# Kernel optimization log

Measured on AMD Instinct MI355X. Metric: run time of the kernel, lower is better.

Reference implementation:

```python
import jax, jax.numpy as jnp
import numpy as np

N_NODES = 50000
N_EDGES = 1600000
N_FEAT = 128
EMB = 128
N_CLASSES = 10
N_GRAPHS = 512


def setup_inputs() -> dict:
    key = jax.random.key(0)
    ks = jax.random.split(key, 12)
    x = jax.random.normal(ks[0], (N_NODES, N_FEAT), dtype=jnp.float32)
    edge_index = jax.random.randint(ks[1], (2, N_EDGES), 0, N_NODES, dtype=jnp.int64)
    batch = jnp.sort(jax.random.randint(ks[2], (N_NODES,), 0, N_GRAPHS, dtype=jnp.int64))
    def glorot(k, fan_in, fan_out):
        lim = jnp.sqrt(6.0 / (fan_in + fan_out)).astype(jnp.float32)
        return jax.random.uniform(k, (fan_in, fan_out), jnp.float32, -lim, lim)
    W0 = glorot(ks[3], N_FEAT, EMB); b0 = jnp.zeros((EMB,), jnp.float32)
    W1 = glorot(ks[4], EMB, EMB);    b1 = jnp.zeros((EMB,), jnp.float32)
    W2 = glorot(ks[5], EMB, EMB);    b2 = jnp.zeros((EMB,), jnp.float32)
    Wout = glorot(ks[6], EMB, N_CLASSES)
    bout = jnp.zeros((N_CLASSES,), jnp.float32)
    return {"x": x, "edge_index": edge_index, "batch": batch,
            "W0": W0, "b0": b0, "W1": W1, "b1": b1, "W2": W2, "b2": b2,
            "Wout": Wout, "bout": bout}


def _gcn_conv(x, W, b, src, dst, norm, n_nodes):
    # PyG GCNConv: h = x @ W; aggregate norm * h[src] into dst; add bias.
    h = x @ W                                  # [N, out]
    msg = h[src] * norm[:, None]               # [E+N, out] gather (incl. self-loops)
    out = jax.ops.segment_sum(msg, dst, num_segments=n_nodes)
    return out + b


def reference(x, edge_index, batch, W0, b0, W1, b1, W2, b2, Wout, bout):
    n_nodes = x.shape[0]
    # add self-loops (GCNConv default add_self_loops=True)
    loops = jnp.arange(n_nodes, dtype=edge_index.dtype)
    src = jnp.concatenate([edge_index[0], loops])
    dst = jnp.concatenate([edge_index[1], loops])
    # symmetric normalization D^{-1/2} (A+I) D^{-1/2}
    deg = jax.ops.segment_sum(jnp.ones_like(dst, dtype=x.dtype), dst,
                              num_segments=n_nodes)
    deg_inv_sqrt = jnp.where(deg > 0, jax.lax.rsqrt(jnp.maximum(deg, 1.0)), 0.0)
    norm = deg_inv_sqrt[src] * deg_inv_sqrt[dst]   # [E+N]
    out = jnp.tanh(_gcn_conv(x, W0, b0, src, dst, norm, n_nodes))
    out = jnp.tanh(_gcn_conv(out, W1, b1, src, dst, norm, n_nodes))
    out = _gcn_conv(out, W2, b2, src, dst, norm, n_nodes)
    # global mean pool over per-node graph ids
    sums = jax.ops.segment_sum(out, batch, num_segments=N_GRAPHS)
    counts = jax.ops.segment_sum(jnp.ones((n_nodes,), out.dtype), batch,
                                 num_segments=N_GRAPHS)
    pooled = sums / jnp.maximum(counts, 1.0)[:, None]   # [G, EMB]
    logits = pooled @ Wout + bout                        # [G, C]
    return jax.nn.log_softmax(logits, axis=1)
```

## Files before the change

### kernel.cpp

```cpp
#include <hip/hip_runtime.h>
#include <math.h>


#define BLK_EDGES 4096
#define MAXB 128
#define ECAP 2048
#define NPB 8
#define WS_STRIDE 136

typedef __attribute__((ext_vector_type(8))) short bf16x8;
typedef __attribute__((ext_vector_type(4))) float f32x4;
typedef __attribute__((ext_vector_type(2))) float f32x2;

static __device__ inline unsigned short f2bf(float f) {
    unsigned u = __float_as_uint(f);
    unsigned r = (u + 0x7FFFu + ((u >> 16) & 1u)) >> 16;
    return (unsigned short)r;
}
static __device__ inline float bf_lo(unsigned u) { return __uint_as_float(u << 16); }
static __device__ inline float bf_hi(unsigned u) { return __uint_as_float(u & 0xFFFF0000u); }
static __device__ inline unsigned char f2fp8(float v) {
    v = fminf(fmaxf(v, -240.f), 240.f);
    int u = __builtin_amdgcn_cvt_pk_fp8_f32(v, v, 0, false);
    return (unsigned char)(u & 0xFF);
}

__global__ __launch_bounds__(256) void blk_hist_prep(const int* __restrict__ dst,
        int* __restrict__ histT, int E, int NBLK, int NB,
        const float* __restrict__ W0, const float* __restrict__ W1,
        const float* __restrict__ W2, unsigned short* __restrict__ wt0,
        unsigned short* __restrict__ wt1, unsigned short* __restrict__ wt2) {
    __shared__ int h[MAXB];
    int blk = blockIdx.x, t = threadIdx.x;
    if (blk >= NBLK) {
        int i = (blk - NBLK) * 256 + t;
        int w = i >> 14, j = i & 16383;
        int k = j >> 7, n2 = j & 127;
        const float* Wp = (w == 0) ? W0 : (w == 1) ? W1 : W2;
        unsigned short* Wt = (w == 0) ? wt0 : (w == 1) ? wt1 : wt2;
        Wt[n2 * 128 + k] = f2bf(Wp[k * 128 + n2]);
        return;
    }
    for (int i = t; i < NB; i += 256) h[i] = 0;
    __syncthreads();
    int lo = blk * BLK_EDGES;
    int hi = min(E, lo + BLK_EDGES);
    for (int i = lo + t; i < hi; i += 256)
        atomicAdd(&h[dst[i] >> 9], 1);
    __syncthreads();
    for (int i = t; i < NB; i += 256) histT[i * NBLK + blk] = h[i];
}

__global__ void scan_block(const int* __restrict__ cnt, int* __restrict__ off,
                           int* __restrict__ bsum, int n) {
    __shared__ int lds[256];
    int t = threadIdx.x;
    int i = blockIdx.x * 256 + t;
    int v = (i < n) ? cnt[i] : 0;
    lds[t] = v;
    __syncthreads();
    for (int d = 1; d < 256; d <<= 1) {
        int add = (t >= d) ? lds[t - d] : 0;
        __syncthreads();
        lds[t] += add;
        __syncthreads();
    }
    if (i < n) off[i] = lds[t] - v;
    if (t == 255) bsum[blockIdx.x] = lds[255];
}

__global__ void scan_top(const int* __restrict__ bsum, int* __restrict__ boff,
                         int nblocks) {
    __shared__ int lds[256];
    int t = threadIdx.x;
    int v = (t < nblocks) ? bsum[t] : 0;
    lds[t] = v;
    __syncthreads();
    for (int d = 1; d < 256; d <<= 1) {
        int add = (t >= d) ? lds[t - d] : 0;
        __syncthreads();
        lds[t] += add;
        __syncthreads();
    }
    if (t < nblocks) boff[t] = lds[t] - v;
}

__global__ __launch_bounds__(256) void scatter_packed(const int* __restrict__ src,
        const int* __restrict__ dst, const int* __restrict__ P,
        const int* __restrict__ boff, unsigned* __restrict__ packed,
        int E, int NBLK, int NB) {
    __shared__ int cur[MAXB];
    int blk = blockIdx.x, t = threadIdx.x;
    for (int i = t; i < NB; i += 256) {
        int idx = i * NBLK + blk;
        cur[i] = P[idx] + boff[idx >> 8];
    }
    __syncthreads();
    int lo = blk * BLK_EDGES;
    int hi = min(E, lo + BLK_EDGES);
    for (int i = lo + t; i < hi; i += 256) {
        int d = dst[i];
        int pos = atomicAdd(&cur[d >> 9], 1);
        packed[pos] = ((unsigned)d << 16) | (unsigned)src[i];
    }
}

__global__ __launch_bounds__(256) void bucket_build(const unsigned* __restrict__ packed,
        const int* __restrict__ P, const int* __restrict__ boff, int* __restrict__ off,
        float* __restrict__ dis, unsigned short* __restrict__ csr16,
        int E, int NBLK, int N, int NB) {
    __shared__ int cnt[512];
    __shared__ int loc[512];
    __shared__ int ps[256];
    int b = blockIdx.x, t = threadIdx.x;
    int i0 = b * NBLK, i1 = (b + 1) * NBLK;
    int start = P[i0] + boff[i0 >> 8];
    int end   = (b == NB - 1) ? E : (P[i1] + boff[i1 >> 8]);
    cnt[t] = 0; cnt[t + 256] = 0;
    __syncthreads();
    for (int i = start + t; i < end; i += 256)
        atomicAdd(&cnt[(packed[i] >> 16) & 511], 1);
    __syncthreads();
    int c0 = cnt[2 * t], c1 = cnt[2 * t + 1];
    ps[t] = c0 + c1;
    __syncthreads();
    for (int d = 1; d < 256; d <<= 1) {
        int add = (t >= d) ? ps[t - d] : 0;
        __syncthreads();
        ps[t] += add;
        __syncthreads();
    }
    int pexcl = ps[t] - (c0 + c1);
    loc[2 * t]     = start + pexcl;
    loc[2 * t + 1] = start + pexcl + c0;
    __syncthreads();
    int node0 = b * 512;
    for (int l = t; l < 512; l += 256) {
        int node = node0 + l;
        if (node < N) {
            off[node] = loc[l];
            dis[node] = rsqrtf((float)cnt[l] + 1.0f);
        }
    }
    if (b == NB - 1 && t == 0) off[N] = E;
    __syncthreads();
    for (int i = start + t; i < end; i += 256) {
        unsigned p = packed[i];
        int l = (p >> 16) & 511;
        int pos = atomicAdd(&loc[l], 1);
        csr16[pos] = (unsigned short)(p & 0xFFFFu);
    }
}

template<int IN_F32>
__global__ __launch_bounds__(128) void gemm_mfma(const void* __restrict__ Av,
        const unsigned short* __restrict__ Wt, const float* __restrict__ dis,
        unsigned char* __restrict__ Hs8, int n) {
    __shared__ unsigned short Ws[128 * WS_STRIDE];
    int t = threadIdx.x;
    for (int i = t; i < 128 * 16; i += 128) {
        int r = i >> 4, j = i & 15;
        uint4 u = ((const uint4*)(Wt + r * 128))[j];
        *(uint4*)&Ws[r * WS_STRIDE + j * 8] = u;
    }
    __syncthreads();

    int wave = t >> 6, lane = t & 63;
    int quad = lane >> 4, l16 = lane & 15;
    int row0 = blockIdx.x * 64 + wave * 32;

    int ra0 = row0 + l16;      if (ra0 >= n) ra0 = n - 1;
    int ra1 = row0 + 16 + l16; if (ra1 >= n) ra1 = n - 1;

    f32x4 acc[2][8];
    const f32x4 z = {0.f, 0.f, 0.f, 0.f};
#pragma unroll
    for (int mi = 0; mi < 2; ++mi)
#pragma unroll
        for (int ni = 0; ni < 8; ++ni) acc[mi][ni] = z;

#pragma unroll
    for (int ks = 0; ks < 4; ++ks) {
        int kof = ks * 32 + quad * 8;
        bf16x8 a0, a1;
        if (IN_F32) {
            const float* A0 = (const float*)Av + (size_t)ra0 * 128 + kof;
            const float* A1 = (const float*)Av + (size_t)ra1 * 128 + kof;
            float4 p0 = ((const float4*)A0)[0], p1 = ((const float4*)A0)[1];
            float4 q0 = ((const float4*)A1)[0], q1 = ((const float4*)A1)[1];
            a0[0] = (short)f2bf(p0.x); a0[1] = (short)f2bf(p0.y);
            a0[2] = (short)f2bf(p0.z); a0[3] = (short)f2bf(p0.w);
            a0[4] = (short)f2bf(p1.x); a0[5] = (short)f2bf(p1.y);
            a0[6] = (short)f2bf(p1.z); a0[7] = (short)f2bf(p1.w);
            a1[0] = (short)f2bf(q0.x); a1[1] = (short)f2bf(q0.y);
            a1[2] = (short)f2bf(q0.z); a1[3] = (short)f2bf(q0.w);
            a1[4] = (short)f2bf(q1.x); a1[5] = (short)f2bf(q1.y);
            a1[6] = (short)f2bf(q1.z); a1[7] = (short)f2bf(q1.w);
        } else {
            a0 = *(const bf16x8*)((const unsigned short*)Av + (size_t)ra0 * 128 + kof);
            a1 = *(const bf16x8*)((const unsigned short*)Av + (size_t)ra1 * 128 + kof);
        }
        bf16x8 b[8];
#pragma unroll
        for (int ni = 0; ni < 8; ++ni)
            b[ni] = *(const bf16x8*)&Ws[(ni * 16 + l16) * WS_STRIDE + kof];
#pragma unroll
        for (int ni = 0; ni < 8; ++ni) {
            acc[0][ni] = __builtin_amdgcn_mfma_f32_16x16x32_bf16(a0, b[ni], acc[0][ni], 0, 0, 0);
            acc[1][ni] = __builtin_amdgcn_mfma_f32_16x16x32_bf16(a1, b[ni], acc[1][ni], 0, 0, 0);
        }
    }
#pragma unroll
    for (int mi = 0; mi < 2; ++mi) {
        int rb = row0 + mi * 16 + quad * 4;
#pragma unroll
        for (int reg = 0; reg < 4; ++reg) {
            int r = rb + reg;
            if (r < n) {
                float dv = dis[r];
#pragma unroll
                for (int ni = 0; ni < 8; ++ni)
                    Hs8[(size_t)r * 128 + ni * 16 + l16] = f2fp8(acc[mi][ni][reg] * dv);
            }
        }
    }
}

template<int DO_TANH>
__global__ __launch_bounds__(256) void aggregate3(const unsigned char* __restrict__ hs,
    const unsigned short* __restrict__ csr, const int* __restrict__ off,
    const float* __restrict__ dis, const float* __restrict__ bias,
    unsigned* __restrict__ outp, int n) {
    __shared__ unsigned short eidx[ECAP];
    int t = threadIdx.x;
    int node0 = blockIdx.x * NPB;
    int b0 = off[node0];
    int topn = node0 + NPB < n ? node0 + NPB : n;
    int bN = off[topn];
    int mblk = bN - b0;
    bool staged = (mblk <= ECAP);
    if (staged)
        for (int i = t; i < mblk; i += 256) eidx[i] = csr[b0 + i];
    __syncthreads();

    int w = t >> 6;
    int lane = t & 63;
    int g = lane >> 4;
    int fq = lane & 15;
    unsigned fob = (unsigned)fq << 3;

    float4 bv0 = ((const float4*)bias)[2 * fq];
    float4 bv1 = ((const float4*)bias)[2 * fq + 1];

    int nodeA = node0 + w * 2;
    int e0 = (nodeA < n) ? off[nodeA] : 0;
    for (int s = 0; s < 2; ++s) {
        int node = nodeA + s;
        if (node >= n) break;
        int e1 = off[node + 1];
        int m = e1 - e0;
        int le0 = e0 - b0;
        uint2 sv = *(const uint2*)(hs + (((unsigned)node) << 7) + fob);

        float a0 = 0.f, a1 = 0.f, a2 = 0.f, a3 = 0.f;
        float a4 = 0.f, a5 = 0.f, a6 = 0.f, a7 = 0.f;
        auto cadd = [&](uint2 v) {
            f32x2 p0 = __builtin_amdgcn_cvt_pk_f32_fp8((int)v.x, false);
            f32x2 p1 = __builtin_amdgcn_cvt_pk_f32_fp8((int)v.x, true);
            f32x2 p2 = __builtin_amdgcn_cvt_pk_f32_fp8((int)v.y, false);
            f32x2 p3 = __builtin_amdgcn_cvt_pk_f32_fp8((int)v.y, true);
            a0 += p0.x; a1 += p0.y; a2 += p1.x; a3 += p1.y;
            a4 += p2.x; a5 += p2.y; a6 += p3.x; a7 += p3.y;
        };
        uint2 va[4], vb[4];
        auto sumB = [&](uint2* v) {
#pragma unroll
            for (int j = 0; j < 4; ++j) cadd(v[j]);
        };
        auto loadL = [&](int i, uint2* v) {
#pragma unroll
            for (int j = 0; j < 4; ++j) {
                int e = i + g + 4 * j;
                uint2 val; val.x = 0u; val.y = 0u;
                if (e < m)
                    val = *(const uint2*)(hs +
                          (((unsigned)eidx[le0 + e]) << 7) + fob);
                v[j] = val;
            }
        };
        auto loadG = [&](int i, uint2* v) {
#pragma unroll
            for (int j = 0; j < 4; ++j) {
                int e = i + g + 4 * j;
                uint2 val; val.x = 0u; val.y = 0u;
                if (e < m)
                    val = *(const uint2*)(hs +
                          (((unsigned)csr[e0 + e]) << 7) + fob);
                v[j] = val;
            }
        };

        int B = (m + 15) >> 4;
        if (B) {
            if (staged) {
                loadL(0, va);
                int k = 1;
                for (; k + 1 < B; k += 2) {
                    loadL(k << 4, vb);       sumB(va);
                    loadL((k + 1) << 4, va); sumB(vb);
                }
                if (k < B) { loadL(k << 4, vb); sumB(va); sumB(vb); }
                else       { sumB(va); }
            } else {
                loadG(0, va);
                int k = 1;
                for (; k + 1 < B; k += 2) {
                    loadG(k << 4, vb);       sumB(va);
                    loadG((k + 1) << 4, va); sumB(vb);
                }
                if (k < B) { loadG(k << 4, vb); sumB(va); sumB(vb); }
                else       { sumB(va); }
            }
        }

        a0 += __shfl_xor(a0, 32, 64); a0 += __shfl_xor(a0, 16, 64);
        a1 += __shfl_xor(a1, 32, 64); a1 += __shfl_xor(a1, 16, 64);
        a2 += __shfl_xor(a2, 32, 64); a2 += __shfl_xor(a2, 16, 64);
        a3 += __shfl_xor(a3, 32, 64); a3 += __shfl_xor(a3, 16, 64);
        a4 += __shfl_xor(a4, 32, 64); a4 += __shfl_xor(a4, 16, 64);
        a5 += __shfl_xor(a5, 32, 64); a5 += __shfl_xor(a5, 16, 64);
        a6 += __shfl_xor(a6, 32, 64); a6 += __shfl_xor(a6, 16, 64);
        a7 += __shfl_xor(a7, 32, 64); a7 += __shfl_xor(a7, 16, 64);

        if (g == 0) {
            cadd(sv);
            float dn = dis[node];
            float o0 = fmaf(dn, a0, bv0.x);
            float o1 = fmaf(dn, a1, bv0.y);
            float o2 = fmaf(dn, a2, bv0.z);
            float o3 = fmaf(dn, a3, bv0.w);
            float o4 = fmaf(dn, a4, bv1.x);
            float o5 = fmaf(dn, a5, bv1.y);
            float o6 = fmaf(dn, a6, bv1.z);
            float o7 = fmaf(dn, a7, bv1.w);
            if (DO_TANH) {
                o0 = tanhf(o0); o1 = tanhf(o1); o2 = tanhf(o2); o3 = tanhf(o3);
                o4 = tanhf(o4); o5 = tanhf(o5); o6 = tanhf(o6); o7 = tanhf(o7);
            }
            uint4 o;
            o.x = (unsigned)f2bf(o0) | ((unsigned)f2bf(o1) << 16);
            o.y = (unsigned)f2bf(o2) | ((unsigned)f2bf(o3) << 16);
            o.z = (unsigned)f2bf(o4) | ((unsigned)f2bf(o5) << 16);
            o.w = (unsigned)f2bf(o6) | ((unsigned)f2bf(o7) << 16);
            *(uint4*)(outp + (size_t)node * 64 + fq * 4) = o;
        }
        e0 = e1;
    }
}

__global__ __launch_bounds__(256) void pool_head(const unsigned* __restrict__ actb,
    const int* __restrict__ batch, const float* __restrict__ Wout,
    const float* __restrict__ bout, float* __restrict__ out, int n, int C) {
    __shared__ float psum[4][128];
    __shared__ float l[16];
    __shared__ float stats[2];
    int g = blockIdx.x;
    int t = threadIdx.x;
    int w = t >> 6;
    int lane = t & 63;
    int lo = 0, hi = n;
    while (lo < hi) { int mid = (lo + hi) >> 1; if (batch[mid] < g) lo = mid + 1; else hi = mid; }
    int lo1 = lo, hi1 = n;
    while (lo1 < hi1) { int mid = (lo1 + hi1) >> 1; if (batch[mid] < g + 1) lo1 = mid + 1; else hi1 = mid; }
    float ax = 0.f, ay = 0.f;
    for (int i = lo + w; i < lo1; i += 4) {
        unsigned v = actb[(size_t)i * 64 + lane];
        ax += bf_lo(v);
        ay += bf_hi(v);
    }
    psum[w][2 * lane]     = ax;
    psum[w][2 * lane + 1] = ay;
    __syncthreads();
    if (w == 0) {
        int cnt = lo1 - lo;
        float inv = 1.0f / (float)(cnt > 0 ? cnt : 1);
        float sx = (psum[0][2 * lane] + psum[1][2 * lane])
                 + (psum[2][2 * lane] + psum[3][2 * lane]);
        float sy = (psum[0][2 * lane + 1] + psum[1][2 * lane + 1])
                 + (psum[2][2 * lane + 1] + psum[3][2 * lane + 1]);
        psum[0][2 * lane]     = sx * inv;
        psum[0][2 * lane + 1] = sy * inv;
    }
    __syncthreads();
    if (t < C) {
        float acc = bout[t];
        for (int f = 0; f < 128; ++f)
            acc = fmaf(psum[0][f], Wout[(size_t)f * C + t], acc);
        l[t] = acc;
    }
    __syncthreads();
    if (t == 0) {
        float m = -1e30f;
        for (int c = 0; c < C; ++c) m = fmaxf(m, l[c]);
        float s = 0.f;
        for (int c = 0; c < C; ++c) s += expf(l[c] - m);
        stats[0] = m;
        stats[1] = logf(s);
    }
    __syncthreads();
    if (t < C) out[(size_t)g * C + t] = l[t] - stats[0] - stats[1];
}

extern "C" void kernel_launch(void* const* d_in, const int* in_sizes, int n_in,
                              void* d_out, int out_size, void* d_ws, size_t ws_size,
                              hipStream_t stream) {
    const float* x     = (const float*)d_in[0];
    const int*   edge  = (const int*)d_in[1];
    const int*   batch = (const int*)d_in[2];
    const float* W0 = (const float*)d_in[3];
    const float* b0 = (const float*)d_in[4];
    const float* W1 = (const float*)d_in[5];
    const float* b1 = (const float*)d_in[6];
    const float* W2 = (const float*)d_in[7];
    const float* b2 = (const float*)d_in[8];
    const float* Wout = (const float*)d_in[9];
    const float* bout = (const float*)d_in[10];
    float* out = (float*)d_out;

    const int N = in_sizes[0] / 128;
    const int E = in_sizes[1] / 2;
    const int C = in_sizes[10];
    const int G = out_size / C;

    const int* src = edge;
    const int* dst = edge + E;

    const int NBLK = (E + BLK_EDGES - 1) / BLK_EDGES;
    const int NB   = (N + 511) / 512;
    const int NBQ  = NB * NBLK;
    const int PREPB = (3 * 16384) / 256;

    char* p = (char*)d_ws;
    auto alloc = [&](size_t bytes) -> void* {
        void* r = (void*)p;
        p += (bytes + 255) & ~(size_t)255;
        return r;
    };
    unsigned char* hs = (unsigned char*)alloc((size_t)N * 128);
    unsigned* actb = (unsigned*)alloc((size_t)N * 128 * 2);
    float* dis    = (float*)alloc((size_t)N * 4);
    int*   off    = (int*)alloc((size_t)(N + 1) * 4);
    int*   P      = (int*)alloc((size_t)(NBQ + 1) * 4);
    int*   bsum   = (int*)alloc(256 * 4);
    int*   boff   = (int*)alloc(256 * 4);
    unsigned* packed = (unsigned*)alloc((size_t)E * 4);
    unsigned short* csr16 = (unsigned short*)alloc((size_t)E * 2);
    unsigned short* wt0 = (unsigned short*)alloc(128 * 128 * 2);
    unsigned short* wt1 = (unsigned short*)alloc(128 * 128 * 2);
    unsigned short* wt2 = (unsigned short*)alloc(128 * 128 * 2);

    const int sb = (NBQ + 255) / 256;

    blk_hist_prep<<<NBLK + PREPB, 256, 0, stream>>>(dst, P, E, NBLK, NB,
                                                    W0, W1, W2, wt0, wt1, wt2);
    scan_block<<<sb, 256, 0, stream>>>(P, P, bsum, NBQ);
    scan_top<<<1, 256, 0, stream>>>(bsum, boff, sb);
    scatter_packed<<<NBLK, 256, 0, stream>>>(src, dst, P, boff, packed, E, NBLK, NB);
    bucket_build<<<NB, 256, 0, stream>>>(packed, P, boff, off, dis, csr16, E, NBLK, N, NB);

    const int gb = (N + 63) / 64;
    const int ab = (N + NPB - 1) / NPB;

    gemm_mfma<1><<<gb, 128, 0, stream>>>(x,    wt0, dis, hs, N);
    aggregate3<1><<<ab, 256, 0, stream>>>(hs, csr16, off, dis, b0, actb, N);
    gemm_mfma<0><<<gb, 128, 0, stream>>>(actb, wt1, dis, hs, N);
    aggregate3<1><<<ab, 256, 0, stream>>>(hs, csr16, off, dis, b1, actb, N);
    gemm_mfma<0><<<gb, 128, 0, stream>>>(actb, wt2, dis, hs, N);
    aggregate3<0><<<ab, 256, 0, stream>>>(hs, csr16, off, dis, b2, actb, N);

    pool_head<<<G, 256, 0, stream>>>(actb, batch, Wout, bout, out, N, C);
}
```

Before: 336.7 us.

## Aggregate one node per wavefront, spread epilogue across lanes, use fast tanh

The aggregation kernel now gives each wavefront a single node (4 nodes per block) instead of looping over two nodes per wave, which doubles the grid size. The epilogue is split across all 64 lanes: each 16-lane group finalises two of the eight feature columns, so lanes no longer sit idle while group 0 does the work. tanhf is replaced with an exp/rcp-based approximation. Together these aim to raise parallelism and cut serial epilogue time, at the cost of more blocks and smaller shared-memory staging per block, plus slightly less accurate tanh.

```diff
diff --git a/kernel.cpp b/kernel.cpp
--- a/kernel.cpp
+++ b/kernel.cpp
@@ -5,7 +5,6 @@
 #define BLK_EDGES 4096
 #define MAXB 128
 #define ECAP 2048
-#define NPB 8
 #define WS_STRIDE 136
 
 typedef __attribute__((ext_vector_type(8))) short bf16x8;
@@ -23,6 +22,12 @@
     v = fminf(fmaxf(v, -240.f), 240.f);
     int u = __builtin_amdgcn_cvt_pk_fp8_f32(v, v, 0, false);
     return (unsigned char)(u & 0xFF);
+}
+static __device__ inline float fast_tanh(float x) {
+    float ax = fabsf(x);
+    float e = __expf(2.0f * ax);
+    float r = fmaf(-2.0f, __builtin_amdgcn_rcpf(e + 1.0f), 1.0f);
+    return copysignf(r, x);
 }
 
 __global__ __launch_bounds__(256) void blk_hist_prep(const int* __restrict__ dst,
@@ -233,129 +238,112 @@
     unsigned* __restrict__ outp, int n) {
     __shared__ unsigned short eidx[ECAP];
     int t = threadIdx.x;
-    int node0 = blockIdx.x * NPB;
+    int node0 = blockIdx.x * 4;
     int b0 = off[node0];
-    int topn = node0 + NPB < n ? node0 + NPB : n;
-    int bN = off[topn];
-    int mblk = bN - b0;
+    int top = node0 + 4 < n ? node0 + 4 : n;
+    int b4 = off[top];
+    int mblk = b4 - b0;
     bool staged = (mblk <= ECAP);
     if (staged)
         for (int i = t; i < mblk; i += 256) eidx[i] = csr[b0 + i];
     __syncthreads();
 
-    int w = t >> 6;
+    int node = node0 + (t >> 6);
+    if (node >= n) return;
     int lane = t & 63;
     int g = lane >> 4;
     int fq = lane & 15;
     unsigned fob = (unsigned)fq << 3;
 
-    float4 bv0 = ((const float4*)bias)[2 * fq];
-    float4 bv1 = ((const float4*)bias)[2 * fq + 1];
-
-    int nodeA = node0 + w * 2;
-    int e0 = (nodeA < n) ? off[nodeA] : 0;
-    for (int s = 0; s < 2; ++s) {
-        int node = nodeA + s;
-        if (node >= n) break;
-        int e1 = off[node + 1];
-        int m = e1 - e0;
-        int le0 = e0 - b0;
-        uint2 sv = *(const uint2*)(hs + (((unsigned)node) << 7) + fob);
-
-        float a0 = 0.f, a1 = 0.f, a2 = 0.f, a3 = 0.f;
-        float a4 = 0.f, a5 = 0.f, a6 = 0.f, a7 = 0.f;
-        auto cadd = [&](uint2 v) {
-            f32x2 p0 = __builtin_amdgcn_cvt_pk_f32_fp8((int)v.x, false);
-            f32x2 p1 = __builtin_amdgcn_cvt_pk_f32_fp8((int)v.x, true);
-            f32x2 p2 = __builtin_amdgcn_cvt_pk_f32_fp8((int)v.y, false);
-            f32x2 p3 = __builtin_amdgcn_cvt_pk_f32_fp8((int)v.y, true);
-            a0 += p0.x; a1 += p0.y; a2 += p1.x; a3 += p1.y;
-            a4 += p2.x; a5 += p2.y; a6 += p3.x; a7 += p3.y;
-        };
-        uint2 va[4], vb[4];
-        auto sumB = [&](uint2* v) {
-#pragma unroll
-            for (int j = 0; j < 4; ++j) cadd(v[j]);
-        };
-        auto loadL = [&](int i, uint2* v) {
-#pragma unroll
-            for (int j = 0; j < 4; ++j) {
-                int e = i + g + 4 * j;
-                uint2 val; val.x = 0u; val.y = 0u;
-                if (e < m)
-                    val = *(const uint2*)(hs +
-                          (((unsigned)eidx[le0 + e]) << 7) + fob);
-                v[j] = val;
+    int e0 = off[node];
+    int e1 = off[node + 1];
+    int le0 = e0 - b0;
+    int m = e1 - e0;
+
+    unsigned sv = *(const unsigned short*)(hs + (((unsigned)node) << 7) + fob + 2 * g);
+
+    float a0 = 0.f, a1 = 0.f, a2 = 0.f, a3 = 0.f;
+    float a4 = 0.f, a5 = 0.f, a6 = 0.f, a7 = 0.f;
+    auto cadd = [&](uint2 v) {
+        f32x2 p0 = __builtin_amdgcn_cvt_pk_f32_fp8((int)v.x, false);
+        f32x2 p1 = __builtin_amdgcn_cvt_pk_f32_fp8((int)v.x, true);
+        f32x2 p2 = __builtin_amdgcn_cvt_pk_f32_fp8((int)v.y, false);
+        f32x2 p3 = __builtin_amdgcn_cvt_pk_f32_fp8((int)v.y, true);
+        a0 += p0.x; a1 += p0.y; a2 += p1.x; a3 += p1.y;
+        a4 += p2.x; a5 += p2.y; a6 += p3.x; a7 += p3.y;
+    };
+    uint2 va[4], vb[4];
+    auto sumB = [&](uint2* v) {
+#pragma unroll
+        for (int j = 0; j < 4; ++j) cadd(v[j]);
+    };
+    auto loadL = [&](int i, uint2* v) {
+#pragma unroll
+        for (int j = 0; j < 4; ++j) {
+            int e = i + g + 4 * j;
+            uint2 val; val.x = 0u; val.y = 0u;
+            if (e < m)
+                val = *(const uint2*)(hs +
+                      (((unsigned)eidx[le0 + e]) << 7) + fob);
+            v[j] = val;
+        }
+    };
+    auto loadG = [&](int i, uint2* v) {
+#pragma unroll
+        for (int j = 0; j < 4; ++j) {
+            int e = i + g + 4 * j;
+            uint2 val; val.x = 0u; val.y = 0u;
+            if (e < m)
+                val = *(const uint2*)(hs +
+                      (((unsigned)csr[e0 + e]) << 7) + fob);
+            v[j] = val;
+        }
+    };
+
+    int B = (m + 15) >> 4;
+    if (B) {
+        if (staged) {
+            loadL(0, va);
+            int k = 1;
+            for (; k + 1 < B; k += 2) {
+                loadL(k << 4, vb);       sumB(va);
+                loadL((k + 1) << 4, va); sumB(vb);
             }
-        };
-        auto loadG = [&](int i, uint2* v) {
-#pragma unroll
-            for (int j = 0; j < 4; ++j) {
-                int e = i + g + 4 * j;
-                uint2 val; val.x = 0u; val.y = 0u;
-                if (e < m)
-                    val = *(const uint2*)(hs +
-                          (((unsigned)csr[e0 + e]) << 7) + fob);
-                v[j] = val;
+            if (k < B) { loadL(k << 4, vb); sumB(va); sumB(vb); }
+            else       { sumB(va); }
+        } else {
+            loadG(0, va);
+            int k = 1;
+            for (; k + 1 < B; k += 2) {
+                loadG(k << 4, vb);       sumB(va);
+                loadG((k + 1) << 4, va); sumB(vb);
             }
-        };
-
-        int B = (m + 15) >> 4;
-        if (B) {
-            if (staged) {
-                loadL(0, va);
-                int k = 1;
-                for (; k + 1 < B; k += 2) {
-                    loadL(k << 4, vb);       sumB(va);
-                    loadL((k + 1) << 4, va); sumB(vb);
-                }
-                if (k < B) { loadL(k << 4, vb); sumB(va); sumB(vb); }
-                else       { sumB(va); }
-            } else {
-                loadG(0, va);
-                int k = 1;
-                for (; k + 1 < B; k += 2) {
-                    loadG(k << 4, vb);       sumB(va);
-                    loadG((k + 1) << 4, va); sumB(vb);
-                }
-                if (k < B) { loadG(k << 4, vb); sumB(va); sumB(vb); }
-                else       { sumB(va); }
-            }
-        }
-
-        a0 += __shfl_xor(a0, 32, 64); a0 += __shfl_xor(a0, 16, 64);
-        a1 += __shfl_xor(a1, 32, 64); a1 += __shfl_xor(a1, 16, 64);
-        a2 += __shfl_xor(a2, 32, 64); a2 += __shfl_xor(a2, 16, 64);
-        a3 += __shfl_xor(a3, 32, 64); a3 += __shfl_xor(a3, 16, 64);
-        a4 += __shfl_xor(a4, 32, 64); a4 += __shfl_xor(a4, 16, 64);
-        a5 += __shfl_xor(a5, 32, 64); a5 += __shfl_xor(a5, 16, 64);
-        a6 += __shfl_xor(a6, 32, 64); a6 += __shfl_xor(a6, 16, 64);
-        a7 += __shfl_xor(a7, 32, 64); a7 += __shfl_xor(a7, 16, 64);
-
-        if (g == 0) {
-            cadd(sv);
-            float dn = dis[node];
-            float o0 = fmaf(dn, a0, bv0.x);
-            float o1 = fmaf(dn, a1, bv0.y);
-            float o2 = fmaf(dn, a2, bv0.z);
-            float o3 = fmaf(dn, a3, bv0.w);
-            float o4 = fmaf(dn, a4, bv1.x);
-            float o5 = fmaf(dn, a5, bv1.y);
-            float o6 = fmaf(dn, a6, bv1.z);
-            float o7 = fmaf(dn, a7, bv1.w);
-            if (DO_TANH) {
-                o0 = tanhf(o0); o1 = tanhf(o1); o2 = tanhf(o2); o3 = tanhf(o3);
-                o4 = tanhf(o4); o5 = tanhf(o5); o6 = tanhf(o6); o7 = tanhf(o7);
-            }
-            uint4 o;
-            o.x = (unsigned)f2bf(o0) | ((unsigned)f2bf(o1) << 16);
-            o.y = (unsigned)f2bf(o2) | ((unsigned)f2bf(o3) << 16);
-            o.z = (unsigned)f2bf(o4) | ((unsigned)f2bf(o5) << 16);
-            o.w = (unsigned)f2bf(o6) | ((unsigned)f2bf(o7) << 16);
-            *(uint4*)(outp + (size_t)node * 64 + fq * 4) = o;
-        }
-        e0 = e1;
-    }
+            if (k < B) { loadG(k << 4, vb); sumB(va); sumB(vb); }
+            else       { sumB(va); }
+        }
+    }
+
+    a0 += __shfl_xor(a0, 32, 64); a0 += __shfl_xor(a0, 16, 64);
+    a1 += __shfl_xor(a1, 32, 64); a1 += __shfl_xor(a1, 16, 64);
+    a2 += __shfl_xor(a2, 32, 64); a2 += __shfl_xor(a2, 16, 64);
+    a3 += __shfl_xor(a3, 32, 64); a3 += __shfl_xor(a3, 16, 64);
+    a4 += __shfl_xor(a4, 32, 64); a4 += __shfl_xor(a4, 16, 64);
+    a5 += __shfl_xor(a5, 32, 64); a5 += __shfl_xor(a5, 16, 64);
+    a6 += __shfl_xor(a6, 32, 64); a6 += __shfl_xor(a6, 16, 64);
+    a7 += __shfl_xor(a7, 32, 64); a7 += __shfl_xor(a7, 16, 64);
+
+    float s0 = (g & 2) ? ((g & 1) ? a6 : a4) : ((g & 1) ? a2 : a0);
+    float s1 = (g & 2) ? ((g & 1) ? a7 : a5) : ((g & 1) ? a3 : a1);
+    f32x2 sf = __builtin_amdgcn_cvt_pk_f32_fp8((int)sv, false);
+    s0 += sf.x;
+    s1 += sf.y;
+    float dn = dis[node];
+    float2 bv = ((const float2*)bias)[fq * 4 + g];
+    float o0 = fmaf(dn, s0, bv.x);
+    float o1 = fmaf(dn, s1, bv.y);
+    if (DO_TANH) { o0 = fast_tanh(o0); o1 = fast_tanh(o1); }
+    unsigned o = (unsigned)f2bf(o0) | ((unsigned)f2bf(o1) << 16);
+    outp[(size_t)node * 64 + fq * 4 + g] = o;
 }
 
 __global__ __launch_bounds__(256) void pool_head(const unsigned* __restrict__ actb,
@@ -469,7 +457,7 @@
     bucket_build<<<NB, 256, 0, stream>>>(packed, P, boff, off, dis, csr16, E, NBLK, N, NB);
 
     const int gb = (N + 63) / 64;
-    const int ab = (N + NPB - 1) / NPB;
+    const int ab = (N + 3) / 4;
 
     gemm_mfma<1><<<gb, 128, 0, stream>>>(x,    wt0, dis, hs, N);
     aggregate3<1><<<ab, 256, 0, stream>>>(hs, csr16, off, dis, b0, actb, N);
```

New measurement: 308.7 us. 8.3% less time.
